# Kernel optimization log

Measured on AMD Instinct MI355X. Metric: run time of the kernel, lower is better.

Reference implementation:

```python
import jax, jax.numpy as jnp
import numpy as np

MARGIN = 9.0  # args.transe_margin
NORM_P = 2    # args.transe_norm

B, E, R, D = 32, 100000, 500, 64


def setup_inputs() -> dict:
    key = jax.random.key(0)
    k1, k2, k3, k4 = jax.random.split(key, 4)
    sub = jax.random.randint(k1, (B, 1), 0, E, dtype=jnp.int64)
    rel = jax.random.randint(k2, (B, 1), 0, R, dtype=jnp.int64)
    emb_e = jax.random.normal(k3, (E, D), dtype=jnp.float32)
    emb_rel = jax.random.normal(k4, (R, D), dtype=jnp.float32)
    return {"sub": sub, "rel": rel, "emb_e": emb_e, "emb_rel": emb_rel}


def reference(sub, rel, emb_e, emb_rel):
    # 'rhs' mode, no dropout (input_drop=0), sigmoid=False
    sub_emb = emb_e[sub[:, 0]]    # (B, D)
    rel_emb = emb_rel[rel[:, 0]]  # (B, D)
    q = sub_emb + rel_emb         # (B, D)
    # broadcast diff against full entity table: (B, E, D)
    diff = q[:, None, :] - emb_e[None, :, :]
    if NORM_P == 2:
        dist = jnp.sqrt(jnp.sum(diff * diff, axis=-1))
    else:
        dist = jnp.sum(jnp.abs(diff), axis=-1)
    return MARGIN - dist  # (B, E)
```

## Files before the change

kernel.cpp:

```cpp
#include <hip/hip_runtime.h>

#define MARGIN 9.0f
#define NB 32
#define NE 100000
#define ND 64
#define BLOCK 256

__global__ __launch_bounds__(BLOCK) void transe_score_kernel(
    const int* __restrict__ sub, const int* __restrict__ rel,
    const float* __restrict__ emb_e, const float* __restrict__ emb_rel,
    float* __restrict__ out)
{
    __shared__ float q[NB][ND];
    __shared__ float qq[NB];

    const int t = threadIdx.x;

    for (int i = t; i < NB * ND; i += BLOCK) {
        const int b = i >> 6, d = i & 63;
        q[b][d] = emb_e[(size_t)sub[b] * ND + d] + emb_rel[(size_t)rel[b] * ND + d];
    }
    __syncthreads();
    if (t < NB) {
        float s = 0.f;
#pragma unroll
        for (int d = 0; d < ND; ++d) { const float v = q[t][d]; s += v * v; }
        qq[t] = s;
    }
    __syncthreads();

    const int e = blockIdx.x * BLOCK + t;
    if (e >= NE) return;

    float4 r[16];
    const float4* rp = (const float4*)(emb_e + (size_t)e * ND);
#pragma unroll
    for (int i = 0; i < 16; ++i) r[i] = rp[i];

    float rr = 0.f;
#pragma unroll
    for (int i = 0; i < 16; ++i)
        rr += r[i].x * r[i].x + r[i].y * r[i].y + r[i].z * r[i].z + r[i].w * r[i].w;

    for (int b = 0; b < NB; ++b) {
        float a0 = 0.f, a1 = 0.f, a2 = 0.f, a3 = 0.f;
#pragma unroll
        for (int i = 0; i < 16; ++i) {
            const float4 qv = *(const float4*)&q[b][4 * i];
            a0 += qv.x * r[i].x;
            a1 += qv.y * r[i].y;
            a2 += qv.z * r[i].z;
            a3 += qv.w * r[i].w;
        }
        const float dot = (a0 + a1) + (a2 + a3);
        float d2 = qq[b] + rr - 2.f * dot;
        d2 = fmaxf(d2, 0.f);
        out[(size_t)b * NE + e] = MARGIN - sqrtf(d2);
    }
}

extern "C" void kernel_launch(void* const* d_in, const int* in_sizes, int n_in,
                              void* d_out, int out_size, void* d_ws, size_t ws_size,
                              hipStream_t stream)
{
    const int*   sub     = (const int*)d_in[0];
    const int*   rel     = (const int*)d_in[1];
    const float* emb_e   = (const float*)d_in[2];
    const float* emb_rel = (const float*)d_in[3];
    float*       out     = (float*)d_out;

    const int grid = (NE + BLOCK - 1) / BLOCK;
    transe_score_kernel<<<grid, BLOCK, 0, stream>>>(sub, rel, emb_e, emb_rel, out);
}
```

Before: 98.77 us.

## Split query prep into separate kernel and split batch across grid y

Moves the query embedding computation (q and its squared norm) into a one-block prep kernel that writes to workspace. The scoring kernel then reads q from global memory as uniform scalar loads instead of shared memory, and drops the per-block redundant gather and syncs. The batch dimension is split over a second grid axis so each block handles 16 queries, doubling block count. The cost is an extra launch and reading each entity row twice.

```diff
diff --git a/kernel.cpp b/kernel.cpp
--- a/kernel.cpp
+++ b/kernel.cpp
@@ -5,32 +5,38 @@
 #define NE 100000
 #define ND 64
 #define BLOCK 256
+#define BSPLIT 2
+#define BPER (NB / BSPLIT)
 
-__global__ __launch_bounds__(BLOCK) void transe_score_kernel(
+__global__ __launch_bounds__(256) void transe_prep(
     const int* __restrict__ sub, const int* __restrict__ rel,
     const float* __restrict__ emb_e, const float* __restrict__ emb_rel,
-    float* __restrict__ out)
+    float* __restrict__ qws)
 {
-    __shared__ float q[NB][ND];
-    __shared__ float qq[NB];
-
+    __shared__ float qs[NB][ND];
     const int t = threadIdx.x;
-
-    for (int i = t; i < NB * ND; i += BLOCK) {
+    for (int i = t; i < NB * ND; i += 256) {
         const int b = i >> 6, d = i & 63;
-        q[b][d] = emb_e[(size_t)sub[b] * ND + d] + emb_rel[(size_t)rel[b] * ND + d];
+        const float v = emb_e[(size_t)sub[b] * ND + d] + emb_rel[(size_t)rel[b] * ND + d];
+        qs[b][d] = v;
+        qws[i] = v;
     }
     __syncthreads();
     if (t < NB) {
         float s = 0.f;
 #pragma unroll
-        for (int d = 0; d < ND; ++d) { const float v = q[t][d]; s += v * v; }
-        qq[t] = s;
+        for (int d = 0; d < ND; ++d) { const float v = qs[t][d]; s += v * v; }
+        qws[NB * ND + t] = s;
     }
-    __syncthreads();
+}
 
-    const int e = blockIdx.x * BLOCK + t;
-    if (e >= NE) return;
+__global__ __launch_bounds__(BLOCK) void transe_score(
+    const float* __restrict__ emb_e, const float* __restrict__ qws,
+    float* __restrict__ out)
+{
+    int e = blockIdx.x * BLOCK + threadIdx.x;
+    const bool valid = (e < NE);
+    if (e >= NE) e = NE - 1;
 
     float4 r[16];
     const float4* rp = (const float4*)(emb_e + (size_t)e * ND);
@@ -42,20 +48,23 @@
     for (int i = 0; i < 16; ++i)
         rr += r[i].x * r[i].x + r[i].y * r[i].y + r[i].z * r[i].z + r[i].w * r[i].w;
 
-    for (int b = 0; b < NB; ++b) {
+    const int b0 = blockIdx.y * BPER;
+#pragma unroll 4
+    for (int bb = 0; bb < BPER; ++bb) {
+        const int b = b0 + bb;
+        const float* __restrict__ q = qws + b * ND;
         float a0 = 0.f, a1 = 0.f, a2 = 0.f, a3 = 0.f;
 #pragma unroll
         for (int i = 0; i < 16; ++i) {
-            const float4 qv = *(const float4*)&q[b][4 * i];
-            a0 += qv.x * r[i].x;
-            a1 += qv.y * r[i].y;
-            a2 += qv.z * r[i].z;
-            a3 += qv.w * r[i].w;
+            a0 = fmaf(q[4 * i + 0], r[i].x, a0);
+            a1 = fmaf(q[4 * i + 1], r[i].y, a1);
+            a2 = fmaf(q[4 * i + 2], r[i].z, a2);
+            a3 = fmaf(q[4 * i + 3], r[i].w, a3);
         }
         const float dot = (a0 + a1) + (a2 + a3);
-        float d2 = qq[b] + rr - 2.f * dot;
+        float d2 = qws[NB * ND + b] + rr - 2.f * dot;
         d2 = fmaxf(d2, 0.f);
-        out[(size_t)b * NE + e] = MARGIN - sqrtf(d2);
+        if (valid) out[(size_t)b * NE + e] = MARGIN - sqrtf(d2);
     }
 }
 
@@ -68,7 +77,10 @@
     const float* emb_e   = (const float*)d_in[2];
     const float* emb_rel = (const float*)d_in[3];
     float*       out     = (float*)d_out;
+    float*       qws     = (float*)d_ws;
 
-    const int grid = (NE + BLOCK - 1) / BLOCK;
-    transe_score_kernel<<<grid, BLOCK, 0, stream>>>(sub, rel, emb_e, emb_rel, out);
+    transe_prep<<<1, 256, 0, stream>>>(sub, rel, emb_e, emb_rel, qws);
+
+    dim3 grid((NE + BLOCK - 1) / BLOCK, BSPLIT);
+    transe_score<<<grid, BLOCK, 0, stream>>>(emb_e, qws, out);
 }
```

Result: faster. 96.79 us (median of 2 runs) (-2.0%).
